# Optimization experiments

Measured on AMD Instinct MI355X. Metric: run time of the kernel, lower is better.

## Reference

```python
import jax, jax.numpy as jnp
import numpy as np


def setup_inputs() -> dict:
    key = jax.random.key(0)
    k1, k2, k3 = jax.random.split(key, 3)
    B, C, T = 16, 256, 1024
    inp = jax.random.normal(k1, (B, C, T), dtype=jnp.float32)
    tgt = jax.random.normal(k2, (B, C, T), dtype=jnp.float32)
    mask = jax.random.uniform(k3, (B, T), dtype=jnp.float32)
    return {"inp": inp, "tgt": tgt, "mask": mask}


def reference(inp, tgt, mask):
    # inp, tgt: (B, C, T); mask: (B, T)
    # permute(0,2,1) -> (B, T, C), then mask along T
    x = jnp.transpose(inp, (0, 2, 1)) * mask[:, :, None]  # (B, T, C)
    y = jnp.transpose(tgt, (0, 2, 1)) * mask[:, :, None]  # (B, T, C)
    xy = jnp.einsum('btc,bsc->bts', x, y)  # (B, T, T)
    xx = jnp.einsum('btc,bsc->bts', x, x)  # (B, T, T)
    yy = jnp.einsum('btc,bsc->bts', y, y)  # (B, T, T)
    similarity = 2.0 * xy / (xx + yy)
    loss = jnp.exp(-similarity)
    return jnp.mean(loss)
```

## Files before the change

kernel.cpp:

```cpp
#include <hip/hip_runtime.h>

constexpr int Bc = 16;
constexpr int Cc = 256;
constexpr int Tc = 1024;

typedef __attribute__((ext_vector_type(16))) float f32x16;

__global__ void zero_out_kernel(float* out) { out[0] = 0.0f; }

__device__ inline unsigned f2fp8(float x) {
    unsigned u = __float_as_uint(x);
    unsigned sign = (u >> 24) & 0x80u;
    unsigned au = u & 0x7fffffffu;
    if (au < 0x3c800000u) {
        float m = __uint_as_float(au) * 512.0f;
        unsigned d = (unsigned)(m + 0.5f);
        return (d > 7u) ? (sign | 0x08u) : (sign | d);
    }
    if (au > 0x43e00000u) au = 0x43e00000u;
    au += 0x7ffffu + ((au >> 20) & 1u);
    unsigned e = (au >> 23) - 120u;
    return sign | (e << 3) | ((au >> 20) & 7u);
}

__global__ __launch_bounds__(256) void convert_fp8_kernel(
    const float* __restrict__ inp, const float* __restrict__ tgt,
    unsigned char* __restrict__ PX, unsigned char* __restrict__ PY,
    float* __restrict__ out)
{
    if (blockIdx.x == 0 && threadIdx.x == 0) out[0] = 0.0f;

    __shared__ float tile[32][132];
    const int gid = blockIdx.x;
    const int a  = gid >> 10;
    const int b  = (gid >> 6) & 15;
    const int cs = (gid >> 3) & 7;
    const int tg = gid & 7;
    const int t0 = tg * 128;
    const int tid = threadIdx.x;

    const float* src = a ? tgt : inp;
    unsigned char* dst = a ? PY : PX;

#pragma unroll
    for (int i = 0; i < 4; ++i) {
        const int c  = i * 8 + (tid >> 5);
        const int t4 = (tid & 31) * 4;
        const float4 v = *(const float4*)&src[((size_t)(b * Cc + cs * 32 + c)) * Tc + t0 + t4];
        tile[c][t4 + 0] = v.x; tile[c][t4 + 1] = v.y;
        tile[c][t4 + 2] = v.z; tile[c][t4 + 3] = v.w;
    }
    __syncthreads();

    const int tb  = tid >> 6;
    const int kh  = (tid >> 5) & 1;
    const int row = tid & 31;
    const int t   = tb * 32 + row;
    unsigned un[4];
#pragma unroll
    for (int q = 0; q < 4; ++q) {
        unsigned wv = 0;
#pragma unroll
        for (int jj = 0; jj < 4; ++jj) {
            const int j  = q * 4 + jj;
            const int cp = kh * 8 + (j & 7) + (j >> 3) * 16;
            wv |= f2fp8(tile[cp][t]) << (jj * 8);
        }
        un[q] = wv;
    }
    const size_t off = ((size_t)((b * 8 + cs) * 32 + tg * 4 + tb)) * 1024
                     + kh * 512 + row * 16;
    *(uint4*)(dst + off) = make_uint4(un[0], un[1], un[2], un[3]);
}

#define GLDS16(g, l) __builtin_amdgcn_global_load_lds(               \
    (__attribute__((address_space(1))) void*)(g),                    \
    (__attribute__((address_space(3))) void*)(l), 16, 0, 0)

#define MF(a, b, c) c = __builtin_amdgcn_mfma_f32_32x32x16_fp8_fp8((a), (b), (c), 0, 0, 0)

__device__ inline float epi_sum(const f32x16& XY, const f32x16& SS) {
    float l = 0.0f;
#pragma unroll
    for (int i = 0; i < 16; ++i) {
        float s = 2.0f * XY[i] / SS[i];
        s = fminf(fmaxf(s, -60.0f), 60.0f);
        l += __expf(-s);
    }
    return l;
}

__global__ __launch_bounds__(256, 2) void jvs_fp8_kernel(
    const unsigned char* __restrict__ PX,
    const unsigned char* __restrict__ PY,
    float* __restrict__ out)
{
    __shared__ __align__(16) unsigned char lds[2][32768];

    const int xcd = blockIdx.x & 7;
    const int idx = blockIdx.x >> 3;
    const int b   = xcd * 2 + (idx >> 6);
    const int r6  = idx & 63;
    const int tb0 = (r6 >> 3) * 4;
    const int sb0 = (r6 & 7) * 4;

    const int tid  = threadIdx.x;
    const int lane = tid & 63;
    const int w    = tid >> 6;
    const int wm   = (w >> 1) * 2;
    const int wn   = (w & 1) * 2;

    const unsigned char* gax = PX + ((size_t)(b * 256 + tb0)) * 1024 + tid * 16;
    const unsigned char* gay = PY + ((size_t)(b * 256 + tb0)) * 1024 + tid * 16;
    const unsigned char* gbx = PX + ((size_t)(b * 256 + sb0)) * 1024 + tid * 16;
    const unsigned char* gby = PY + ((size_t)(b * 256 + sb0)) * 1024 + tid * 16;

    const int fo = (lane >> 5) * 512 + (lane & 31) * 16;

    f32x16 z;
#pragma unroll
    for (int i = 0; i < 16; ++i) z[i] = 0.0f;
    f32x16 xy00 = z, xy01 = z, xy10 = z, xy11 = z;
    f32x16 ss00 = z, ss01 = z, ss10 = z, ss11 = z;

#define STAGE64(bufi, cs2)                                            \
    do {                                                              \
        unsigned char* L = lds[bufi];                                 \
        const size_t o0 = (size_t)(cs2) * 2 * 32768;                  \
        const size_t o1 = o0 + 32768;                                 \
        GLDS16(gax + o0, L +     0 + tid * 16);                       \
        GLDS16(gax + o1, L +  4096 + tid * 16);                       \
        GLDS16(gay + o0, L +  8192 + tid * 16);                       \
        GLDS16(gay + o1, L + 12288 + tid * 16);                       \
        GLDS16(gbx + o0, L + 16384 + tid * 16);                       \
        GLDS16(gbx + o1, L + 20480 + tid * 16);                       \
        GLDS16(gby + o0, L + 24576 + tid * 16);                       \
        GLDS16(gby + o1, L + 28672 + tid * 16);                       \
    } while (0)

    STAGE64(0, 0);
    __syncthreads();

    for (int it = 0; it < 4; ++it) {
        if (it < 3) STAGE64((it + 1) & 1, it + 1);
        const unsigned char* L = lds[it & 1];

#pragma unroll
        for (int h = 0; h < 2; ++h) {
            const int ho = h * 4096;
            const long2 ax0 = *(const long2*)&L[ho +         (wm + 0) * 1024 + fo];
            const long2 ax1 = *(const long2*)&L[ho +         (wm + 1) * 1024 + fo];
            const long2 ay0 = *(const long2*)&L[ho +  8192 + (wm + 0) * 1024 + fo];
            const long2 ay1 = *(const long2*)&L[ho +  8192 + (wm + 1) * 1024 + fo];
            const long2 bx0 = *(const long2*)&L[ho + 16384 + (wn + 0) * 1024 + fo];
            const long2 bx1 = *(const long2*)&L[ho + 16384 + (wn + 1) * 1024 + fo];
            const long2 by0 = *(const long2*)&L[ho + 24576 + (wn + 0) * 1024 + fo];
            const long2 by1 = *(const long2*)&L[ho + 24576 + (wn + 1) * 1024 + fo];

            MF(ax0.x, bx0.x, ss00); MF(ax0.x, bx1.x, ss01);
            MF(ax1.x, bx0.x, ss10); MF(ax1.x, bx1.x, ss11);
            MF(ay0.x, by0.x, ss00); MF(ay0.x, by1.x, ss01);
            MF(ay1.x, by0.x, ss10); MF(ay1.x, by1.x, ss11);
            MF(ax0.x, by0.x, xy00); MF(ax0.x, by1.x, xy01);
            MF(ax1.x, by0.x, xy10); MF(ax1.x, by1.x, xy11);
            MF(ax0.y, bx0.y, ss00); MF(ax0.y, bx1.y, ss01);
            MF(ax1.y, bx0.y, ss10); MF(ax1.y, bx1.y, ss11);
            MF(ay0.y, by0.y, ss00); MF(ay0.y, by1.y, ss01);
            MF(ay1.y, by0.y, ss10); MF(ay1.y, by1.y, ss11);
            MF(ax0.y, by0.y, xy00); MF(ax0.y, by1.y, xy01);
            MF(ax1.y, by0.y, xy10); MF(ax1.y, by1.y, xy11);
        }

        __syncthreads();
    }
#undef STAGE64

    float local = epi_sum(xy00, ss00) + epi_sum(xy01, ss01)
                + epi_sum(xy10, ss10) + epi_sum(xy11, ss11);

#pragma unroll
    for (int off = 32; off > 0; off >>= 1)
        local += __shfl_down(local, off, 64);

    float* red = (float*)lds;
    if (lane == 0) red[w] = local;
    __syncthreads();
    if (tid == 0)
        atomicAdd(out, (red[0] + red[1] + red[2] + red[3])
                       * (1.0f / ((float)Bc * (float)Tc * (float)Tc)));
}

constexpr int TILE = 64;
constexpr int KC   = 16;

__global__ __launch_bounds__(256) void jvs_loss_kernel(
    const float* __restrict__ inp, const float* __restrict__ tgt, float* __restrict__ out)
{
    __shared__ float xs_t[KC][TILE];
    __shared__ float xs_s[KC][TILE];
    __shared__ float ys_t[KC][TILE];
    __shared__ float ys_s[KC][TILE];

    constexpr int NT = Tc / TILE;
    const int blk = blockIdx.x;
    const int b   = blk / (NT * NT);
    const int r   = blk % (NT * NT);
    const int t0  = (r / NT) * TILE;
    const int s0  = (r % NT) * TILE;
    const int tid = threadIdx.x;
    const int tx  = tid & 15;
    const int ty  = tid >> 4;
    const int lrow  = tid >> 4;
    const int lcol4 = tid & 15;
    const float* baseI = inp + (size_t)b * Cc * Tc;
    const float* baseT = tgt + (size_t)b * Cc * Tc;

    float acc_xy[4][4] = {{0.f}}, acc_xx[4][4] = {{0.f}}, acc_yy[4][4] = {{0.f}};
    for (int c0 = 0; c0 < Cc; c0 += KC) {
        __syncthreads();
        const size_t rowOff = (size_t)(c0 + lrow) * Tc;
        *(float4*)&xs_t[lrow][lcol4 * 4] = *(const float4*)(baseI + rowOff + t0 + lcol4 * 4);
        *(float4*)&xs_s[lrow][lcol4 * 4] = *(const float4*)(baseI + rowOff + s0 + lcol4 * 4);
        *(float4*)&ys_t[lrow][lcol4 * 4] = *(const float4*)(baseT + rowOff + t0 + lcol4 * 4);
        *(float4*)&ys_s[lrow][lcol4 * 4] = *(const float4*)(baseT + rowOff + s0 + lcol4 * 4);
        __syncthreads();
#pragma unroll
        for (int kc = 0; kc < KC; ++kc) {
            float xt[4], xsv[4], yt[4], ysv[4];
#pragma unroll
            for (int i = 0; i < 4; ++i) {
                xt[i]  = xs_t[kc][ty * 4 + i];  yt[i]  = ys_t[kc][ty * 4 + i];
                xsv[i] = xs_s[kc][tx * 4 + i];  ysv[i] = ys_s[kc][tx * 4 + i];
            }
#pragma unroll
            for (int i = 0; i < 4; ++i)
#pragma unroll
                for (int j = 0; j < 4; ++j) {
                    acc_xy[i][j] += xt[i] * ysv[j];
                    acc_xx[i][j] += xt[i] * xsv[j];
                    acc_yy[i][j] += yt[i] * ysv[j];
                }
        }
    }
    float local = 0.0f;
#pragma unroll
    for (int i = 0; i < 4; ++i)
#pragma unroll
        for (int j = 0; j < 4; ++j) {
            float sim = 2.0f * acc_xy[i][j] / (acc_xx[i][j] + acc_yy[i][j]);
            sim = fminf(fmaxf(sim, -60.0f), 60.0f);
            local += __expf(-sim);
        }
#pragma unroll
    for (int off = 32; off > 0; off >>= 1) local += __shfl_down(local, off, 64);
    __shared__ float red[4];
    if ((tid & 63) == 0) red[tid >> 6] = local;
    __syncthreads();
    if (tid == 0)
        atomicAdd(out, (red[0] + red[1] + red[2] + red[3])
                       * (1.0f / ((float)Bc * (float)Tc * (float)Tc)));
}

extern "C" void kernel_launch(void* const* d_in, const int* in_sizes, int n_in,
                              void* d_out, int out_size, void* d_ws, size_t ws_size,
                              hipStream_t stream) {
    const float* inp = (const float*)d_in[0];
    const float* tgt = (const float*)d_in[1];
    float* out = (float*)d_out;

    const size_t oneP = (size_t)Bc * Cc * Tc;
    if (ws_size >= 2 * oneP) {
        unsigned char* PX = (unsigned char*)d_ws;
        unsigned char* PY = PX + oneP;
        convert_fp8_kernel<<<2048, 256, 0, stream>>>(inp, tgt, PX, PY, out);
        jvs_fp8_kernel<<<1024, 256, 0, stream>>>(PX, PY, out);
    } else {
        zero_out_kernel<<<1, 1, 0, stream>>>(out);
        jvs_loss_kernel<<<Bc * (Tc / TILE) * (Tc / TILE), 256, 0, stream>>>(inp, tgt, out);
    }
}
```

Before: 104.4 us.

## Load fp8 MFMA operands directly from global memory instead of LDS staging

```diff
diff --git a/kernel.cpp b/kernel.cpp
--- a/kernel.cpp
+++ b/kernel.cpp
@@ -73,10 +73,6 @@
     *(uint4*)(dst + off) = make_uint4(un[0], un[1], un[2], un[3]);
 }
 
-#define GLDS16(g, l) __builtin_amdgcn_global_load_lds(               \
-    (__attribute__((address_space(1))) void*)(g),                    \
-    (__attribute__((address_space(3))) void*)(l), 16, 0, 0)
-
 #define MF(a, b, c) c = __builtin_amdgcn_mfma_f32_32x32x16_fp8_fp8((a), (b), (c), 0, 0, 0)
 
 __device__ inline float epi_sum(const f32x16& XY, const f32x16& SS) {
@@ -95,8 +91,6 @@
     const unsigned char* __restrict__ PY,
     float* __restrict__ out)
 {
-    __shared__ __align__(16) unsigned char lds[2][32768];
-
     const int xcd = blockIdx.x & 7;
     const int idx = blockIdx.x >> 3;
     const int b   = xcd * 2 + (idx >> 6);
@@ -110,12 +104,16 @@
     const int wm   = (w >> 1) * 2;
     const int wn   = (w & 1) * 2;
 
-    const unsigned char* gax = PX + ((size_t)(b * 256 + tb0)) * 1024 + tid * 16;
-    const unsigned char* gay = PY + ((size_t)(b * 256 + tb0)) * 1024 + tid * 16;
-    const unsigned char* gbx = PX + ((size_t)(b * 256 + sb0)) * 1024 + tid * 16;
-    const unsigned char* gby = PY + ((size_t)(b * 256 + sb0)) * 1024 + tid * 16;
-
     const int fo = (lane >> 5) * 512 + (lane & 31) * 16;
+
+    const unsigned char* pax0 = PX + ((size_t)(b * 256 + tb0 + wm + 0)) * 1024 + fo;
+    const unsigned char* pax1 = PX + ((size_t)(b * 256 + tb0 + wm + 1)) * 1024 + fo;
+    const unsigned char* pay0 = PY + ((size_t)(b * 256 + tb0 + wm + 0)) * 1024 + fo;
+    const unsigned char* pay1 = PY + ((size_t)(b * 256 + tb0 + wm + 1)) * 1024 + fo;
+    const unsigned char* pbx0 = PX + ((size_t)(b * 256 + sb0 + wn + 0)) * 1024 + fo;
+    const unsigned char* pbx1 = PX + ((size_t)(b * 256 + sb0 + wn + 1)) * 1024 + fo;
+    const unsigned char* pby0 = PY + ((size_t)(b * 256 + sb0 + wn + 0)) * 1024 + fo;
+    const unsigned char* pby1 = PY + ((size_t)(b * 256 + sb0 + wn + 1)) * 1024 + fo;
 
     f32x16 z;
 #pragma unroll
@@ -123,57 +121,31 @@
     f32x16 xy00 = z, xy01 = z, xy10 = z, xy11 = z;
     f32x16 ss00 = z, ss01 = z, ss10 = z, ss11 = z;
 
-#define STAGE64(bufi, cs2)                                            \
-    do {                                                              \
-        unsigned char* L = lds[bufi];                                 \
-        const size_t o0 = (size_t)(cs2) * 2 * 32768;                  \
-        const size_t o1 = o0 + 32768;                                 \
-        GLDS16(gax + o0, L +     0 + tid * 16);                       \
-        GLDS16(gax + o1, L +  4096 + tid * 16);                       \
-        GLDS16(gay + o0, L +  8192 + tid * 16);                       \
-        GLDS16(gay + o1, L + 12288 + tid * 16);                       \
-        GLDS16(gbx + o0, L + 16384 + tid * 16);                       \
-        GLDS16(gbx + o1, L + 20480 + tid * 16);                       \
-        GLDS16(gby + o0, L + 24576 + tid * 16);                       \
-        GLDS16(gby + o1, L + 28672 + tid * 16);                       \
-    } while (0)
-
-    STAGE64(0, 0);
-    __syncthreads();
-
-    for (int it = 0; it < 4; ++it) {
-        if (it < 3) STAGE64((it + 1) & 1, it + 1);
-        const unsigned char* L = lds[it & 1];
-
-#pragma unroll
-        for (int h = 0; h < 2; ++h) {
-            const int ho = h * 4096;
-            const long2 ax0 = *(const long2*)&L[ho +         (wm + 0) * 1024 + fo];
-            const long2 ax1 = *(const long2*)&L[ho +         (wm + 1) * 1024 + fo];
-            const long2 ay0 = *(const long2*)&L[ho +  8192 + (wm + 0) * 1024 + fo];
-            const long2 ay1 = *(const long2*)&L[ho +  8192 + (wm + 1) * 1024 + fo];
-            const long2 bx0 = *(const long2*)&L[ho + 16384 + (wn + 0) * 1024 + fo];
-            const long2 bx1 = *(const long2*)&L[ho + 16384 + (wn + 1) * 1024 + fo];
-            const long2 by0 = *(const long2*)&L[ho + 24576 + (wn + 0) * 1024 + fo];
-            const long2 by1 = *(const long2*)&L[ho + 24576 + (wn + 1) * 1024 + fo];
-
-            MF(ax0.x, bx0.x, ss00); MF(ax0.x, bx1.x, ss01);
-            MF(ax1.x, bx0.x, ss10); MF(ax1.x, bx1.x, ss11);
-            MF(ay0.x, by0.x, ss00); MF(ay0.x, by1.x, ss01);
-            MF(ay1.x, by0.x, ss10); MF(ay1.x, by1.x, ss11);
-            MF(ax0.x, by0.x, xy00); MF(ax0.x, by1.x, xy01);
-            MF(ax1.x, by0.x, xy10); MF(ax1.x, by1.x, xy11);
-            MF(ax0.y, bx0.y, ss00); MF(ax0.y, bx1.y, ss01);
-            MF(ax1.y, bx0.y, ss10); MF(ax1.y, bx1.y, ss11);
-            MF(ay0.y, by0.y, ss00); MF(ay0.y, by1.y, ss01);
-            MF(ay1.y, by0.y, ss10); MF(ay1.y, by1.y, ss11);
-            MF(ax0.y, by0.y, xy00); MF(ax0.y, by1.y, xy01);
-            MF(ax1.y, by0.y, xy10); MF(ax1.y, by1.y, xy11);
-        }
-
-        __syncthreads();
-    }
-#undef STAGE64
+#pragma unroll
+    for (int cs = 0; cs < 8; ++cs) {
+        const size_t o = (size_t)cs * 32768;
+        const long2 ax0 = *(const long2*)(pax0 + o);
+        const long2 ax1 = *(const long2*)(pax1 + o);
+        const long2 ay0 = *(const long2*)(pay0 + o);
+        const long2 ay1 = *(const long2*)(pay1 + o);
+        const long2 bx0 = *(const long2*)(pbx0 + o);
+        const long2 bx1 = *(const long2*)(pbx1 + o);
+        const long2 by0 = *(const long2*)(pby0 + o);
+        const long2 by1 = *(const long2*)(pby1 + o);
+
+        MF(ax0.x, bx0.x, ss00); MF(ax0.x, bx1.x, ss01);
+        MF(ax1.x, bx0.x, ss10); MF(ax1.x, bx1.x, ss11);
+        MF(ay0.x, by0.x, ss00); MF(ay0.x, by1.x, ss01);
+        MF(ay1.x, by0.x, ss10); MF(ay1.x, by1.x, ss11);
+        MF(ax0.x, by0.x, xy00); MF(ax0.x, by1.x, xy01);
+        MF(ax1.x, by0.x, xy10); MF(ax1.x, by1.x, xy11);
+        MF(ax0.y, bx0.y, ss00); MF(ax0.y, bx1.y, ss01);
+        MF(ax1.y, bx0.y, ss10); MF(ax1.y, bx1.y, ss11);
+        MF(ay0.y, by0.y, ss00); MF(ay0.y, by1.y, ss01);
+        MF(ay1.y, by0.y, ss10); MF(ay1.y, by1.y, ss11);
+        MF(ax0.y, by0.y, xy00); MF(ax0.y, by1.y, xy01);
+        MF(ax1.y, by0.y, xy10); MF(ax1.y, by1.y, xy11);
+    }
 
     float local = epi_sum(xy00, ss00) + epi_sum(xy01, ss01)
                 + epi_sum(xy10, ss10) + epi_sum(xy11, ss11);
@@ -182,7 +154,7 @@
     for (int off = 32; off > 0; off >>= 1)
         local += __shfl_down(local, off, 64);
 
-    float* red = (float*)lds;
+    __shared__ float red[4];
     if (lane == 0) red[w] = local;
     __syncthreads();
     if (tid == 0)
```

New measurement: 105.3 us. Within noise of the previous version (+0.8%).
